# Performance work log

Measured on AMD Instinct MI355X. Metric: run time of the kernel, lower is better.

## Reference

```python
import jax, jax.numpy as jnp
import numpy as np

N, E = 50000, 600000
D_IN = 128; D_HID = 128; D_OUT = 128
HEADS = 4; HD = D_HID // HEADS  # per-head dim (32); also edge-encoder output dim
EDGE_DIM = 64


def _w(key, shape, scale=0.05):
    return jax.random.normal(key, shape, dtype=jnp.float32) * scale


def setup_inputs() -> dict:
    key = jax.random.key(0)
    ks = jax.random.split(key, 20)
    return {
        "x": jax.random.normal(ks[0], (N, D_IN), dtype=jnp.float32),
        "edge_index": jax.random.randint(ks[1], (2, E), 0, N),
        "edge_attr": jax.random.normal(ks[2], (E, EDGE_DIM), dtype=jnp.float32),
        # edge feature encoders: Linear(EDGE_DIM, HD), one per GNN layer
        "ew0": _w(ks[3], (EDGE_DIM, HD)), "eb0": jnp.zeros((HD,), jnp.float32),
        "ew1": _w(ks[4], (EDGE_DIM, HD)), "eb1": jnp.zeros((HD,), jnp.float32),
        # ordered-message-passing attention: Linear(dim, 1) per layer
        "ow0": _w(ks[5], (D_IN, 1)), "ob0": jnp.zeros((1,), jnp.float32),
        "ow1": _w(ks[6], (D_OUT, 1)), "ob1": jnp.zeros((1,), jnp.float32),
        # GATConv layer 0: in=D_IN, heads=HEADS, per-head out=HD, edge_dim=HD
        "g0_W": _w(ks[7], (D_IN, HEADS * HD)),
        "g0_as": _w(ks[8], (HEADS, HD)), "g0_ad": _w(ks[9], (HEADS, HD)),
        "g0_We": _w(ks[10], (HD, HEADS * HD)), "g0_ae": _w(ks[11], (HEADS, HD)),
        "g0_b": jnp.zeros((HEADS * HD,), jnp.float32),
        # GATConv layer 1 (final): in=HEADS*HD, heads=1, out=D_OUT, edge_dim=HD
        "g1_W": _w(ks[12], (HEADS * HD, D_OUT)),
        "g1_as": _w(ks[13], (1, D_OUT)), "g1_ad": _w(ks[14], (1, D_OUT)),
        "g1_We": _w(ks[15], (HD, D_OUT)), "g1_ae": _w(ks[16], (1, D_OUT)),
        "g1_b": jnp.zeros((D_OUT,), jnp.float32),
    }


def _gat_conv(x, src, dst, e_attr, W, a_src, a_dst, We, a_e, bias):
    """PyG GATConv with edge features, add_self_loops=True, fill_value='mean'."""
    H, C = a_src.shape
    n = x.shape[0]
    # self-loop edge_attr = per-dst mean of incoming edge_attr (PyG fill_value='mean')
    ones = jnp.ones((src.shape[0],), x.dtype)
    cnt = jax.ops.segment_sum(ones, dst, num_segments=n)
    loop_attr = jax.ops.segment_sum(e_attr, dst, num_segments=n) / jnp.maximum(cnt, 1.0)[:, None]
    loop = jnp.arange(n)
    src2 = jnp.concatenate([src, loop])
    dst2 = jnp.concatenate([dst, loop])
    ea2 = jnp.concatenate([e_attr, loop_attr], axis=0)  # [E+N, HD]
    xs = (x @ W).reshape(n, H, C)                       # [N, H, C]
    al_src = jnp.einsum('nhc,hc->nh', xs, a_src)
    al_dst = jnp.einsum('nhc,hc->nh', xs, a_dst)
    ee = (ea2 @ We).reshape(-1, H, C)                   # [E+N, H, C]
    al_e = jnp.einsum('ehc,hc->eh', ee, a_e)
    alpha = jax.nn.leaky_relu(al_src[src2] + al_dst[dst2] + al_e, 0.2)  # [E+N, H]
    # segment softmax over edges sharing a destination node
    mx = jax.ops.segment_max(alpha, dst2, num_segments=n)
    ex = jnp.exp(alpha - mx[dst2])
    den = jax.ops.segment_sum(ex, dst2, num_segments=n)
    coef = ex / (den[dst2] + 1e-16)
    out = jax.ops.segment_sum(xs[src2] * coef[..., None], dst2, num_segments=n)
    return out.reshape(n, H * C) + bias


def reference(x, edge_index, edge_attr, ew0, eb0, ew1, eb1, ow0, ob0, ow1, ob1,
              g0_W, g0_as, g0_ad, g0_We, g0_ae, g0_b,
              g1_W, g1_as, g1_ad, g1_We, g1_ae, g1_b):
    src, dst = edge_index[0], edge_index[1]
    original_x = x
    layers = [
        (ew0, eb0, ow0, ob0, g0_W, g0_as, g0_ad, g0_We, g0_ae, g0_b),
        (ew1, eb1, ow1, ob1, g1_W, g1_as, g1_ad, g1_We, g1_ae, g1_b),
    ]
    for i, (ew, eb, ow, ob, W, a_s, a_d, We, a_e, b) in enumerate(layers):
        te = jax.nn.relu(edge_attr @ ew + eb)            # [E, HD]
        score = (x @ ow + ob)[:, 0]                       # [N] order-attention scores
        te = te * jnp.exp(score)[src][:, None]            # ordered message weighting
        x_new = _gat_conv(x, src, dst, te, W, a_s, a_d, We, a_e, b)
        x = x_new + x if x.shape[-1] == x_new.shape[-1] else x_new
        if i < len(layers) - 1:
            x = jax.nn.relu(x)  # dropout p=0.0 in eval
    if original_x.shape[-1] == x.shape[-1]:
        x = x + original_x
    return x
```

## Files before the change

### kernel.cpp

```cpp
#include <hip/hip_runtime.h>
#include <math.h>

#define D 128
#define ED 64
#define HD 32

typedef short s16x8 __attribute__((ext_vector_type(8)));
typedef unsigned short u16x8 __attribute__((ext_vector_type(8)));
typedef float f32x4 __attribute__((ext_vector_type(4)));

static __device__ inline unsigned short f2b(float f) {
  unsigned int u = __float_as_uint(f);
  unsigned int r = (u + 0x7fff + ((u >> 16) & 1)) >> 16;
  return (unsigned short)r;
}
static __device__ inline float b2f(unsigned short b) {
  return __uint_as_float(((unsigned int)b) << 16);
}

__global__ __launch_bounds__(256)
void count_prep_kernel(const int* __restrict__ dst, int* __restrict__ cnt,
                       int* __restrict__ rank, int E, int egrid,
                       const float* __restrict__ g0W, unsigned short* __restrict__ Wt0,
                       const float* __restrict__ g1W, unsigned short* __restrict__ Wt1,
                       const float* __restrict__ ew0, unsigned short* __restrict__ ewt0,
                       const float* __restrict__ ew1, unsigned short* __restrict__ ewt1,
                       const float* __restrict__ g0We, const float* __restrict__ g0ae,
                       float* __restrict__ M0,
                       const float* __restrict__ g1We, const float* __restrict__ g1ae,
                       float* __restrict__ M1) {
  int b = blockIdx.x, t = threadIdx.x;
  if (b < egrid) {
    int e = b * 256 + t;
    if (e < E) rank[e] = atomicAdd(&cnt[dst[e]], 1);
    return;
  }
  int pb = b - egrid;
  if (pb < 128) {
    const float* W = pb < 64 ? g0W : g1W;
    unsigned short* Wt = pb < 64 ? Wt0 : Wt1;
    int id = (pb & 63) * 256 + t;
    int nn = id >> 7, k = id & 127;
    Wt[id] = f2b(W[k * D + nn]);
  } else if (pb < 144) {
    const float* ew = pb < 136 ? ew0 : ew1;
    unsigned short* ewt = pb < 136 ? ewt0 : ewt1;
    int id = ((pb - 128) & 7) * 256 + t;
    if (id < HD * ED) {
      int i = id >> 6, k = id & 63;
      int ch = (i < 16) ? ((i >> 2) * 8 + (i & 3))
                        : (((i - 16) >> 2) * 8 + 4 + ((i - 16) & 3));
      ewt[id] = f2b(ew[k * HD + ch]);
    }
  } else if (pb == 144) {
    if (t < HD * 4) {
      int d = t >> 2, h = t & 3;
      float s = 0.f;
      for (int c = 0; c < 32; ++c) s += g0We[d * D + h * 32 + c] * g0ae[h * 32 + c];
      M0[t] = s;
    }
  } else {
    if (t < HD) {
      float s = 0.f;
      for (int c = 0; c < D; ++c) s += g1We[t * D + c] * g1ae[c];
      M1[t] = s;
    }
  }
}

__global__ __launch_bounds__(256)
void scan_a_kernel(const int* __restrict__ cnt, int* __restrict__ bsum, int n) {
  __shared__ int sh[256];
  int t = threadIdx.x;
  int i = blockIdx.x * 256 + t;
  sh[t] = (i < n) ? cnt[i] : 0;
  __syncthreads();
  for (int off = 128; off >= 1; off >>= 1) {
    if (t < off) sh[t] += sh[t + off];
    __syncthreads();
  }
  if (t == 0) bsum[blockIdx.x] = sh[0];
}

__global__ __launch_bounds__(256)
void scan_b_kernel(const int* __restrict__ bsum, int* __restrict__ boff, int nb,
                   int* __restrict__ rowptr_n, int E) {
  __shared__ int sh[256];
  int t = threadIdx.x;
  int v = (t < nb) ? bsum[t] : 0;
  sh[t] = v;
  __syncthreads();
  for (int off = 1; off < 256; off <<= 1) {
    int add = (t >= off) ? sh[t - off] : 0;
    __syncthreads();
    sh[t] += add;
    __syncthreads();
  }
  if (t < nb) boff[t] = sh[t] - v;
  if (t == 0) *rowptr_n = E;
}

__global__ __launch_bounds__(256)
void scan_c_kernel(const int* __restrict__ cnt, const int* __restrict__ boff,
                   int* __restrict__ rowptr, int n) {
  __shared__ int sh[256];
  int t = threadIdx.x;
  int i = blockIdx.x * 256 + t;
  int v = (i < n) ? cnt[i] : 0;
  sh[t] = v;
  __syncthreads();
  for (int off = 1; off < 256; off <<= 1) {
    int add = (t >= off) ? sh[t - off] : 0;
    __syncthreads();
    sh[t] += add;
    __syncthreads();
  }
  if (i < n) rowptr[i] = boff[blockIdx.x] + sh[t] - v;
}

template<int H, bool INBF16>
static __device__ void gemm_body(int gblk, int tid, const void* xin,
                                 const unsigned short* __restrict__ Wt,
                                 const float* __restrict__ a_s, const float* __restrict__ a_d,
                                 const float* __restrict__ ow, const float* __restrict__ ob,
                                 unsigned short* __restrict__ xs, float* __restrict__ al_src,
                                 float* __restrict__ al_dst, float* __restrict__ escore,
                                 float2* __restrict__ als1, int n) {
  int wave = tid >> 6;
  int lane = tid & 63;
  int q = lane >> 4;
  int l16 = lane & 15;
  int base = gblk * 64 + wave * 16;
  int rowRaw = base + l16;
  int row = rowRaw < n ? rowRaw : n - 1;
  s16x8 a[4];
  float scp = 0.f;
  if (INBF16) {
    const unsigned short* xrow = (const unsigned short*)xin + (size_t)row * D;
#pragma unroll
    for (int kk = 0; kk < 4; ++kk) {
      int kb = kk * 32 + q * 8;
      u16x8 v = *(const u16x8*)(xrow + kb);
      float4 o0 = *(const float4*)(ow + kb);
      float4 o1 = *(const float4*)(ow + kb + 4);
      scp += b2f(v[0]) * o0.x + b2f(v[1]) * o0.y + b2f(v[2]) * o0.z + b2f(v[3]) * o0.w
           + b2f(v[4]) * o1.x + b2f(v[5]) * o1.y + b2f(v[6]) * o1.z + b2f(v[7]) * o1.w;
      a[kk] = *(const s16x8*)&v;
    }
  } else {
    const float* xrow = (const float*)xin + (size_t)row * D;
#pragma unroll
    for (int kk = 0; kk < 4; ++kk) {
      int kb = kk * 32 + q * 8;
      float4 v0 = *(const float4*)(xrow + kb);
      float4 v1 = *(const float4*)(xrow + kb + 4);
      float4 o0 = *(const float4*)(ow + kb);
      float4 o1 = *(const float4*)(ow + kb + 4);
      scp += v0.x * o0.x + v0.y * o0.y + v0.z * o0.z + v0.w * o0.w
           + v1.x * o1.x + v1.y * o1.y + v1.z * o1.z + v1.w * o1.w;
      s16x8 t;
      t[0] = (short)f2b(v0.x); t[1] = (short)f2b(v0.y);
      t[2] = (short)f2b(v0.z); t[3] = (short)f2b(v0.w);
      t[4] = (short)f2b(v1.x); t[5] = (short)f2b(v1.y);
      t[6] = (short)f2b(v1.z); t[7] = (short)f2b(v1.w);
      a[kk] = t;
    }
  }
  scp += __shfl_xor(scp, 16);
  scp += __shfl_xor(scp, 32);
  if (H == 4) {
    if (q == 0 && rowRaw < n) escore[rowRaw] = __expf(scp + ob[0]);
  }

  f32x4 acc[8];
#pragma unroll
  for (int nf = 0; nf < 8; ++nf) { f32x4 z = {0.f, 0.f, 0.f, 0.f}; acc[nf] = z; }
#pragma unroll
  for (int kk = 0; kk < 4; ++kk) {
    int kb = kk * 32 + q * 8;
#pragma unroll
    for (int nf = 0; nf < 8; ++nf) {
      s16x8 b = *(const s16x8*)(Wt + (size_t)(nf * 16 + l16) * D + kb);
      acc[nf] = __builtin_amdgcn_mfma_f32_16x16x32_bf16(a[kk], b, acc[nf], 0, 0, 0);
    }
  }
#pragma unroll
  for (int nf = 0; nf < 8; ++nf) {
#pragma unroll
    for (int r = 0; r < 4; ++r) {
      int rr = base + q * 4 + r;
      if (rr < n) xs[(size_t)rr * D + nf * 16 + l16] = f2b(acc[nf][r]);
    }
  }
  float asv[8], adv[8];
#pragma unroll
  for (int nf = 0; nf < 8; ++nf) { asv[nf] = a_s[nf * 16 + l16]; adv[nf] = a_d[nf * 16 + l16]; }
  if (H == 4) {
    float mys = 0.f, myd = 0.f;
#pragma unroll
    for (int r = 0; r < 4; ++r) {
#pragma unroll
      for (int h = 0; h < 4; ++h) {
        float vs = acc[2 * h][r] * asv[2 * h] + acc[2 * h + 1][r] * asv[2 * h + 1];
        float vd = acc[2 * h][r] * adv[2 * h] + acc[2 * h + 1][r] * adv[2 * h + 1];
        vs += __shfl_xor(vs, 1); vd += __shfl_xor(vd, 1);
        vs += __shfl_xor(vs, 2); vd += __shfl_xor(vd, 2);
        vs += __shfl_xor(vs, 4); vd += __shfl_xor(vd, 4);
        vs += __shfl_xor(vs, 8); vd += __shfl_xor(vd, 8);
        if (l16 == r * 4 + h) { mys = vs; myd = vd; }
      }
    }
    int orow = base + q * 4 + (l16 >> 2);
    if (orow < n) {
      al_src[(size_t)orow * 4 + (l16 & 3)] = mys;
      al_dst[(size_t)orow * 4 + (l16 & 3)] = myd;
    }
  } else {
    float mys = 0.f, myd = 0.f;
#pragma unroll
    for (int r = 0; r < 4; ++r) {
      float vs = 0.f, vd = 0.f;
#pragma unroll
      for (int nf = 0; nf < 8; ++nf) { vs = fmaf(acc[nf][r], asv[nf], vs); vd = fmaf(acc[nf][r], adv[nf], vd); }
      vs += __shfl_xor(vs, 1); vd += __shfl_xor(vd, 1);
      vs += __shfl_xor(vs, 2); vd += __shfl_xor(vd, 2);
      vs += __shfl_xor(vs, 4); vd += __shfl_xor(vd, 4);
      vs += __shfl_xor(vs, 8); vd += __shfl_xor(vd, 8);
      if (l16 == r) { mys = vs; myd = vd; }
    }
    float scr = __shfl(scp, q * 4 + l16);
    int orow = base + q * 4 + l16;
    if (l16 < 4 && orow < n) {
      al_dst[orow] = myd;
      als1[orow] = make_float2(mys, __expf(scr + ob[0]));
    }
  }
}

__global__ __launch_bounds__(256)
void fill_gemm_kernel(const int* __restrict__ src, const int* __restrict__ dst,
                      const int* __restrict__ rowptr, const int* __restrict__ rank,
                      int2* __restrict__ slotmap, int E, int fgrid,
                      const float* __restrict__ x, const unsigned short* __restrict__ Wt0,
                      const float* __restrict__ g0as, const float* __restrict__ g0ad,
                      const float* __restrict__ ow0, const float* __restrict__ ob0,
                      unsigned short* __restrict__ xs, float* __restrict__ al_src,
                      float* __restrict__ al_dst, float* __restrict__ escore, int n) {
  if ((int)blockIdx.x < fgrid) {
    int e = blockIdx.x * 256 + threadIdx.x;
    if (e < E) {
      int d = dst[e];
      slotmap[rowptr[d] + rank[e]] = make_int2(e, src[e]);
    }
  } else {
    gemm_body<4, false>(blockIdx.x - fgrid, threadIdx.x, x, Wt0, g0as, g0ad, ow0, ob0,
                        xs, al_src, al_dst, escore, nullptr, n);
  }
}

__global__ __launch_bounds__(256)
void gemm1_kernel(const unsigned short* __restrict__ x1b, const unsigned short* __restrict__ Wt,
                  const float* __restrict__ a_s, const float* __restrict__ a_d,
                  const float* __restrict__ ow, const float* __restrict__ ob,
                  unsigned short* __restrict__ xs, float* __restrict__ al_dst,
                  float2* __restrict__ als1, int n) {
  gemm_body<1, true>(blockIdx.x, threadIdx.x, x1b, Wt, a_s, a_d, ow, ob,
                     xs, nullptr, al_dst, nullptr, als1, n);
}

__global__ __launch_bounds__(256)
void edge_csr_kernel(const int2* __restrict__ slotmap,
                     const float* __restrict__ ea,
                     const unsigned short* __restrict__ ewt0p,
                     const unsigned short* __restrict__ ewt1p,
                     const float* __restrict__ eb0, const float* __restrict__ eb1,
                     const float* __restrict__ M0, const float* __restrict__ M1,
                     const float* __restrict__ escore0,
                     float* __restrict__ alef0,
                     float* __restrict__ ale1raw,
                     int E) {
  int wave = threadIdx.x >> 6, lane = threadIdx.x & 63;
  int q = lane >> 4, l16 = lane & 15;
  int ebase = (blockIdx.x * 4 + wave) * 64;
  if (ebase >= E) return;
  s16x8 a0l0 = *(const s16x8*)(ewt0p + l16 * 64 + q * 8);
  s16x8 a0l1 = *(const s16x8*)(ewt0p + l16 * 64 + 32 + q * 8);
  s16x8 a0h0 = *(const s16x8*)(ewt0p + (16 + l16) * 64 + q * 8);
  s16x8 a0h1 = *(const s16x8*)(ewt0p + (16 + l16) * 64 + 32 + q * 8);
  s16x8 a1l0 = *(const s16x8*)(ewt1p + l16 * 64 + q * 8);
  s16x8 a1l1 = *(const s16x8*)(ewt1p + l16 * 64 + 32 + q * 8);
  s16x8 a1h0 = *(const s16x8*)(ewt1p + (16 + l16) * 64 + q * 8);
  s16x8 a1h1 = *(const s16x8*)(ewt1p + (16 + l16) * 64 + 32 + q * 8);
  float4 b0lo = *(const float4*)(eb0 + q * 8);
  float4 b0hi = *(const float4*)(eb0 + q * 8 + 4);
  float4 b1lo = *(const float4*)(eb1 + q * 8);
  float4 b1hi = *(const float4*)(eb1 + q * 8 + 4);
  s16x8 mf0, mf1;
#pragma unroll
  for (int j = 0; j < 8; ++j) {
    mf0[j] = (l16 < 4) ? (short)f2b(M0[(q * 8 + j) * 4 + l16]) : (short)0;
    mf1[j] = (l16 == 0) ? (short)f2b(M1[q * 8 + j]) : (short)0;
  }
  int el = ebase + lane;
  int elc = el < E ? el : E - 1;
  int2 sm = slotmap[elc];
  int eo = sm.x;
  float esc = escore0[sm.y];

#pragma unroll
  for (int st = 0; st < 4; ++st) {
    int slot16 = st * 16 + l16;
    int e16 = ebase + slot16;
    int row = __shfl(eo, slot16);
    const float* er = ea + (size_t)row * ED;
    float4 u0 = *(const float4*)(er + q * 8);
    float4 u1 = *(const float4*)(er + q * 8 + 4);
    float4 u2 = *(const float4*)(er + 32 + q * 8);
    float4 u3 = *(const float4*)(er + 32 + q * 8 + 4);
    s16x8 bk0, bk1;
    bk0[0] = (short)f2b(u0.x); bk0[1] = (short)f2b(u0.y);
    bk0[2] = (short)f2b(u0.z); bk0[3] = (short)f2b(u0.w);
    bk0[4] = (short)f2b(u1.x); bk0[5] = (short)f2b(u1.y);
    bk0[6] = (short)f2b(u1.z); bk0[7] = (short)f2b(u1.w);
    bk1[0] = (short)f2b(u2.x); bk1[1] = (short)f2b(u2.y);
    bk1[2] = (short)f2b(u2.z); bk1[3] = (short)f2b(u2.w);
    bk1[4] = (short)f2b(u3.x); bk1[5] = (short)f2b(u3.y);
    bk1[6] = (short)f2b(u3.z); bk1[7] = (short)f2b(u3.w);
    f32x4 zl0 = {0.f,0.f,0.f,0.f}, zh0 = {0.f,0.f,0.f,0.f};
    f32x4 zl1 = {0.f,0.f,0.f,0.f}, zh1 = {0.f,0.f,0.f,0.f};
    zl0 = __builtin_amdgcn_mfma_f32_16x16x32_bf16(a0l0, bk0, zl0, 0, 0, 0);
    zl0 = __builtin_amdgcn_mfma_f32_16x16x32_bf16(a0l1, bk1, zl0, 0, 0, 0);
    zh0 = __builtin_amdgcn_mfma_f32_16x16x32_bf16(a0h0, bk0, zh0, 0, 0, 0);
    zh0 = __builtin_amdgcn_mfma_f32_16x16x32_bf16(a0h1, bk1, zh0, 0, 0, 0);
    zl1 = __builtin_amdgcn_mfma_f32_16x16x32_bf16(a1l0, bk0, zl1, 0, 0, 0);
    zl1 = __builtin_amdgcn_mfma_f32_16x16x32_bf16(a1l1, bk1, zl1, 0, 0, 0);
    zh1 = __builtin_amdgcn_mfma_f32_16x16x32_bf16(a1h0, bk0, zh1, 0, 0, 0);
    zh1 = __builtin_amdgcn_mfma_f32_16x16x32_bf16(a1h1, bk1, zh1, 0, 0, 0);
    s16x8 zb0, zb1;
    zb0[0] = (short)f2b(fmaxf(zl0[0] + b0lo.x, 0.f));
    zb0[1] = (short)f2b(fmaxf(zl0[1] + b0lo.y, 0.f));
    zb0[2] = (short)f2b(fmaxf(zl0[2] + b0lo.z, 0.f));
    zb0[3] = (short)f2b(fmaxf(zl0[3] + b0lo.w, 0.f));
    zb0[4] = (short)f2b(fmaxf(zh0[0] + b0hi.x, 0.f));
    zb0[5] = (short)f2b(fmaxf(zh0[1] + b0hi.y, 0.f));
    zb0[6] = (short)f2b(fmaxf(zh0[2] + b0hi.z, 0.f));
    zb0[7] = (short)f2b(fmaxf(zh0[3] + b0hi.w, 0.f));
    zb1[0] = (short)f2b(fmaxf(zl1[0] + b1lo.x, 0.f));
    zb1[1] = (short)f2b(fmaxf(zl1[1] + b1lo.y, 0.f));
    zb1[2] = (short)f2b(fmaxf(zl1[2] + b1lo.z, 0.f));
    zb1[3] = (short)f2b(fmaxf(zl1[3] + b1lo.w, 0.f));
    zb1[4] = (short)f2b(fmaxf(zh1[0] + b1hi.x, 0.f));
    zb1[5] = (short)f2b(fmaxf(zh1[1] + b1hi.y, 0.f));
    zb1[6] = (short)f2b(fmaxf(zh1[2] + b1hi.z, 0.f));
    zb1[7] = (short)f2b(fmaxf(zh1[3] + b1hi.w, 0.f));
    f32x4 r0 = {0.f,0.f,0.f,0.f}, r1 = {0.f,0.f,0.f,0.f};
    r0 = __builtin_amdgcn_mfma_f32_16x16x32_bf16(mf0, zb0, r0, 0, 0, 0);
    r1 = __builtin_amdgcn_mfma_f32_16x16x32_bf16(mf1, zb1, r1, 0, 0, 0);
    float esc_e = __shfl(esc, slot16);
    if (q == 0 && e16 < E) {
      *(float4*)(alef0 + (size_t)e16 * 4) =
          make_float4(r0[0] * esc_e, r0[1] * esc_e, r0[2] * esc_e, r0[3] * esc_e);
      ale1raw[e16] = r1[0];
    }
  }
}

template<int H, bool RELU, bool ADD_ORIG, bool INBF16, bool OUTBF16>
__global__ __launch_bounds__(256)
void agg_kernel(const int* __restrict__ rowptr, const int2* __restrict__ slotmap,
                const unsigned short* __restrict__ xs, const float* __restrict__ alef,
                const float* __restrict__ al_src, const float* __restrict__ al_dst,
                const float2* __restrict__ als1,
                const float* __restrict__ bias, const void* __restrict__ xin,
                const float* __restrict__ orig, void* __restrict__ outv, int n) {
  int wid = blockIdx.x * 4 + (threadIdx.x >> 6);
  int lane = threadIdx.x & 63;
  if (wid >= n) return;
  int half = lane >> 5;
  int l32 = lane & 31;
  int h0 = (H == 4) ? (l32 >> 3) : 0;
  const ushort4* xs4 = (const ushort4*)xs;
  float adst = al_dst[(size_t)wid * H + h0];
  float ax0 = 0.f, ax1 = 0.f, ax2 = 0.f, ax3 = 0.f, den = 0.f, sale = 0.f;
  int b = rowptr[wid], e = rowptr[wid + 1];
  int m = e - b;

#define EDGE_ACC(I_)                                                     \
  {                                                                      \
    int idx_ = (I_);                                                     \
    bool v_ = idx_ < e;                                                  \
    int ic_ = v_ ? idx_ : b;                                             \
    int s_ = slotmap[ic_].y;                                             \
    float al_, ev_;                                                      \
    if (H == 4) {                                                        \
      al_ = alef[(size_t)ic_ * 4 + h0];                                  \
      float aa_ = al_src[(size_t)s_ * 4 + h0] + adst + al_;              \
      ev_ = __expf(aa_ > 0.f ? aa_ : 0.2f * aa_);                        \
    } else {                                                             \
      float2 ae_ = als1[s_];                                             \
      al_ = alef[ic_] * ae_.y;                                           \
      float aa_ = ae_.x + adst + al_;                                    \
      ev_ = __expf(aa_ > 0.f ? aa_ : 0.2f * aa_);                        \
    }                                                                    \
    if (!v_) { ev_ = 0.f; al_ = 0.f; }                                   \
    ushort4 u_ = xs4[(size_t)s_ * 32 + l32];                             \
    ax0 = fmaf(ev_, b2f(u_.x), ax0); ax1 = fmaf(ev_, b2f(u_.y), ax1);    \
    ax2 = fmaf(ev_, b2f(u_.z), ax2); ax3 = fmaf(ev_, b2f(u_.w), ax3);    \
    den += ev_; sale += al_;                                             \
  }

  for (int k = 0; k < m; k += 8) {
    int i0 = b + k + half;
    EDGE_ACC(i0)
    EDGE_ACC(i0 + 2)
    EDGE_ACC(i0 + 4)
    EDGE_ACC(i0 + 6)
  }
#undef EDGE_ACC

  ax0 += __shfl_xor(ax0, 32); ax1 += __shfl_xor(ax1, 32);
  ax2 += __shfl_xor(ax2, 32); ax3 += __shfl_xor(ax3, 32);
  den += __shfl_xor(den, 32); sale += __shfl_xor(sale, 32);

  float la = sale / (float)(m > 1 ? m : 1);
  float asrc_w = (H == 4) ? al_src[(size_t)wid * 4 + h0] : als1[wid].x;
  float a = asrc_w + adst + la;
  float lr = a > 0.f ? a : 0.2f * a;
  float evl = __expf(lr);
  ushort4 us = xs4[(size_t)wid * 32 + l32];
  ax0 = fmaf(evl, b2f(us.x), ax0); ax1 = fmaf(evl, b2f(us.y), ax1);
  ax2 = fmaf(evl, b2f(us.z), ax2); ax3 = fmaf(evl, b2f(us.w), ax3);
  float dinv = 1.f / (den + evl + 1e-16f);
  if (half == 0) {
    float4 bi = ((const float4*)bias)[l32];
    float o0 = ax0 * dinv + bi.x;
    float o1 = ax1 * dinv + bi.y;
    float o2 = ax2 * dinv + bi.z;
    float o3 = ax3 * dinv + bi.w;
    if (INBF16) {
      ushort4 xi = ((const ushort4*)xin)[(size_t)wid * 32 + l32];
      o0 += b2f(xi.x); o1 += b2f(xi.y); o2 += b2f(xi.z); o3 += b2f(xi.w);
    } else {
      float4 xi = ((const float4*)xin)[(size_t)wid * 32 + l32];
      o0 += xi.x; o1 += xi.y; o2 += xi.z; o3 += xi.w;
    }
    if (ADD_ORIG) {
      float4 og = ((const float4*)orig)[(size_t)wid * 32 + l32];
      o0 += og.x; o1 += og.y; o2 += og.z; o3 += og.w;
    }
    if (RELU) {
      o0 = fmaxf(o0, 0.f); o1 = fmaxf(o1, 0.f);
      o2 = fmaxf(o2, 0.f); o3 = fmaxf(o3, 0.f);
    }
    if (OUTBF16) {
      ushort4 ob;
      ob.x = f2b(o0); ob.y = f2b(o1); ob.z = f2b(o2); ob.w = f2b(o3);
      ((ushort4*)outv)[(size_t)wid * 32 + l32] = ob;
    } else {
      ((float4*)outv)[(size_t)wid * 32 + l32] = make_float4(o0, o1, o2, o3);
    }
  }
}

extern "C" void kernel_launch(void* const* d_in, const int* in_sizes, int n_in,
                              void* d_out, int out_size, void* d_ws, size_t ws_size,
                              hipStream_t stream) {
  const float* x   = (const float*)d_in[0];
  const int*   ei  = (const int*)d_in[1];
  const float* ea  = (const float*)d_in[2];
  const float* ew0 = (const float*)d_in[3];
  const float* eb0 = (const float*)d_in[4];
  const float* ew1 = (const float*)d_in[5];
  const float* eb1 = (const float*)d_in[6];
  const float* ow0 = (const float*)d_in[7];
  const float* ob0 = (const float*)d_in[8];
  const float* ow1 = (const float*)d_in[9];
  const float* ob1 = (const float*)d_in[10];
  const float* g0W = (const float*)d_in[11];
  const float* g0as= (const float*)d_in[12];
  const float* g0ad= (const float*)d_in[13];
  const float* g0We= (const float*)d_in[14];
  const float* g0ae= (const float*)d_in[15];
  const float* g0b = (const float*)d_in[16];
  const float* g1W = (const float*)d_in[17];
  const float* g1as= (const float*)d_in[18];
  const float* g1ad= (const float*)d_in[19];
  const float* g1We= (const float*)d_in[20];
  const float* g1ae= (const float*)d_in[21];
  const float* g1b = (const float*)d_in[22];
  float* out = (float*)d_out;

  const int N = in_sizes[0] / D;
  const int E = in_sizes[1] / 2;
  const int* srcp = ei;
  const int* dstp = ei + E;

  char* w = (char*)d_ws;
  size_t off = 0;
  auto alloc = [&](size_t bytes) {
    void* p = w + off;
    off += (bytes + 255) & ~(size_t)255;
    return p;
  };
  size_t Nb = ((size_t)N * 4 + 255) & ~(size_t)255;
  int*   cnt     = (int*)alloc(Nb);
  int*   rank    = (int*)alloc((size_t)E * 4);
  unsigned short* xs   = (unsigned short*)alloc((size_t)N * D * 2);
  unsigned short* x1b  = (unsigned short*)alloc((size_t)N * D * 2);
  float* alef0   = (float*)alloc((size_t)E * 4 * 4);
  float* ale1raw = (float*)alloc((size_t)E * 4);
  float* al_src  = (float*)alloc((size_t)N * 4 * 4);
  float* al_dst  = (float*)alloc((size_t)N * 4 * 4);
  float* escore  = (float*)alloc((size_t)N * 4);
  float2* als1   = (float2*)alloc((size_t)N * 8);
  float* M0      = (float*)alloc(HD * 4 * 4);
  float* M1      = (float*)alloc(HD * 4);
  unsigned short* Wt0 = (unsigned short*)alloc((size_t)D * D * 2);
  unsigned short* Wt1 = (unsigned short*)alloc((size_t)D * D * 2);
  unsigned short* ewt0 = (unsigned short*)alloc((size_t)HD * ED * 2);
  unsigned short* ewt1 = (unsigned short*)alloc((size_t)HD * ED * 2);
  int*   rowptr  = (int*)alloc((size_t)(N + 1) * 4);
  int2*  slotmap = (int2*)alloc((size_t)E * 8);
  int*   bsum    = (int*)alloc(1024);
  int*   boff    = (int*)alloc(1024);

  int egrid  = (E + 255) / 256;
  int ngrid4 = (N + 3) / 4;
  int ggrid  = (N + 63) / 64;
  int nsb    = (N + 255) / 256;

  hipMemsetAsync(cnt, 0, Nb, stream);
  count_prep_kernel<<<egrid + 146, 256, 0, stream>>>(dstp, cnt, rank, E, egrid,
                                                     g0W, Wt0, g1W, Wt1,
                                                     ew0, ewt0, ew1, ewt1,
                                                     g0We, g0ae, M0, g1We, g1ae, M1);
  scan_a_kernel<<<nsb, 256, 0, stream>>>(cnt, bsum, N);
  scan_b_kernel<<<1, 256, 0, stream>>>(bsum, boff, nsb, rowptr + N, E);
  scan_c_kernel<<<nsb, 256, 0, stream>>>(cnt, boff, rowptr, N);
  fill_gemm_kernel<<<egrid + ggrid, 256, 0, stream>>>(srcp, dstp, rowptr, rank,
                                                      slotmap, E, egrid,
                                                      x, Wt0, g0as, g0ad, ow0, ob0,
                                                      xs, al_src, al_dst, escore, N);
  edge_csr_kernel<<<egrid, 256, 0, stream>>>(slotmap, ea, ewt0, ewt1,
                                             eb0, eb1, M0, M1, escore,
                                             alef0, ale1raw, E);
  agg_kernel<4, true, false, false, true><<<ngrid4, 256, 0, stream>>>(
      rowptr, slotmap, xs, alef0, al_src, al_dst, nullptr,
      g0b, x, nullptr, x1b, N);
  gemm1_kernel<<<ggrid, 256, 0, stream>>>(x1b, Wt1, g1as, g1ad, ow1, ob1,
                                          xs, al_dst, als1, N);
  agg_kernel<1, false, true, true, false><<<ngrid4, 256, 0, stream>>>(
      rowptr, slotmap, xs, ale1raw, nullptr, al_dst, als1,
      g1b, x1b, x, out, N);
}
```

Measured before the change: 222.9 us.

## Fuse CSR fill, layer-0 GEMM and edge encoder into one kernel

Moves the layer-0 order-attention score computation into the count/prep kernel so it is ready earlier. The edge encoder then processes edges in original order, reading src directly instead of going through the slotmap. That removes its dependency on the CSR fill and lets it be merged with the fill and GEMM into a single launch. The aggregation kernel now looks up per-edge attention values through the original edge id stored in slotmap, which adds one indirect gather per edge there. In exchange it saves a kernel launch and allows the edge_attr rows to be read sequentially.

Result: slower. 233.8 us (+4.9%).

```diff
diff --git a/kernel.cpp b/kernel.cpp
--- a/kernel.cpp
+++ b/kernel.cpp
@@ -28,7 +28,9 @@
                        const float* __restrict__ g0We, const float* __restrict__ g0ae,
                        float* __restrict__ M0,
                        const float* __restrict__ g1We, const float* __restrict__ g1ae,
-                       float* __restrict__ M1) {
+                       float* __restrict__ M1,
+                       const float* __restrict__ x, const float* __restrict__ ow0,
+                       const float* __restrict__ ob0, float* __restrict__ escore, int n) {
   int b = blockIdx.x, t = threadIdx.x;
   if (b < egrid) {
     int e = b * 256 + t;
@@ -59,11 +61,21 @@
       for (int c = 0; c < 32; ++c) s += g0We[d * D + h * 32 + c] * g0ae[h * 32 + c];
       M0[t] = s;
     }
-  } else {
+  } else if (pb == 145) {
     if (t < HD) {
       float s = 0.f;
       for (int c = 0; c < D; ++c) s += g1We[t * D + c] * g1ae[c];
       M1[t] = s;
+    }
+  } else {
+    int node = (pb - 146) * 4 + (t >> 6);
+    int lane = t & 63;
+    if (node < n) {
+      const float* xr = x + (size_t)node * D;
+      float s = xr[lane] * ow0[lane] + xr[64 + lane] * ow0[64 + lane];
+#pragma unroll
+      for (int off = 32; off >= 1; off >>= 1) s += __shfl_xor(s, off);
+      if (lane == 0) escore[node] = __expf(s + ob0[0]);
     }
   }
 }
@@ -124,7 +136,7 @@
                                  const float* __restrict__ a_s, const float* __restrict__ a_d,
                                  const float* __restrict__ ow, const float* __restrict__ ob,
                                  unsigned short* __restrict__ xs, float* __restrict__ al_src,
-                                 float* __restrict__ al_dst, float* __restrict__ escore,
+                                 float* __restrict__ al_dst,
                                  float2* __restrict__ als1, int n) {
   int wave = tid >> 6;
   int lane = tid & 63;
@@ -141,10 +153,12 @@
     for (int kk = 0; kk < 4; ++kk) {
       int kb = kk * 32 + q * 8;
       u16x8 v = *(const u16x8*)(xrow + kb);
-      float4 o0 = *(const float4*)(ow + kb);
-      float4 o1 = *(const float4*)(ow + kb + 4);
-      scp += b2f(v[0]) * o0.x + b2f(v[1]) * o0.y + b2f(v[2]) * o0.z + b2f(v[3]) * o0.w
-           + b2f(v[4]) * o1.x + b2f(v[5]) * o1.y + b2f(v[6]) * o1.z + b2f(v[7]) * o1.w;
+      if (H == 1) {
+        float4 o0 = *(const float4*)(ow + kb);
+        float4 o1 = *(const float4*)(ow + kb + 4);
+        scp += b2f(v[0]) * o0.x + b2f(v[1]) * o0.y + b2f(v[2]) * o0.z + b2f(v[3]) * o0.w
+             + b2f(v[4]) * o1.x + b2f(v[5]) * o1.y + b2f(v[6]) * o1.z + b2f(v[7]) * o1.w;
+      }
       a[kk] = *(const s16x8*)&v;
     }
   } else {
@@ -154,10 +168,12 @@
       int kb = kk * 32 + q * 8;
       float4 v0 = *(const float4*)(xrow + kb);
       float4 v1 = *(const float4*)(xrow + kb + 4);
-      float4 o0 = *(const float4*)(ow + kb);
-      float4 o1 = *(const float4*)(ow + kb + 4);
-      scp += v0.x * o0.x + v0.y * o0.y + v0.z * o0.z + v0.w * o0.w
-           + v1.x * o1.x + v1.y * o1.y + v1.z * o1.z + v1.w * o1.w;
+      if (H == 1) {
+        float4 o0 = *(const float4*)(ow + kb);
+        float4 o1 = *(const float4*)(ow + kb + 4);
+        scp += v0.x * o0.x + v0.y * o0.y + v0.z * o0.z + v0.w * o0.w
+             + v1.x * o1.x + v1.y * o1.y + v1.z * o1.z + v1.w * o1.w;
+      }
       s16x8 t;
       t[0] = (short)f2b(v0.x); t[1] = (short)f2b(v0.y);
       t[2] = (short)f2b(v0.z); t[3] = (short)f2b(v0.w);
@@ -166,10 +182,9 @@
       a[kk] = t;
     }
   }
-  scp += __shfl_xor(scp, 16);
-  scp += __shfl_xor(scp, 32);
-  if (H == 4) {
-    if (q == 0 && rowRaw < n) escore[rowRaw] = __expf(scp + ob[0]);
+  if (H == 1) {
+    scp += __shfl_xor(scp, 16);
+    scp += __shfl_xor(scp, 32);
   }
 
   f32x4 acc[8];
@@ -237,51 +252,20 @@
   }
 }
 
-__global__ __launch_bounds__(256)
-void fill_gemm_kernel(const int* __restrict__ src, const int* __restrict__ dst,
-                      const int* __restrict__ rowptr, const int* __restrict__ rank,
-                      int2* __restrict__ slotmap, int E, int fgrid,
-                      const float* __restrict__ x, const unsigned short* __restrict__ Wt0,
-                      const float* __restrict__ g0as, const float* __restrict__ g0ad,
-                      const float* __restrict__ ow0, const float* __restrict__ ob0,
-                      unsigned short* __restrict__ xs, float* __restrict__ al_src,
-                      float* __restrict__ al_dst, float* __restrict__ escore, int n) {
-  if ((int)blockIdx.x < fgrid) {
-    int e = blockIdx.x * 256 + threadIdx.x;
-    if (e < E) {
-      int d = dst[e];
-      slotmap[rowptr[d] + rank[e]] = make_int2(e, src[e]);
-    }
-  } else {
-    gemm_body<4, false>(blockIdx.x - fgrid, threadIdx.x, x, Wt0, g0as, g0ad, ow0, ob0,
-                        xs, al_src, al_dst, escore, nullptr, n);
-  }
-}
-
-__global__ __launch_bounds__(256)
-void gemm1_kernel(const unsigned short* __restrict__ x1b, const unsigned short* __restrict__ Wt,
-                  const float* __restrict__ a_s, const float* __restrict__ a_d,
-                  const float* __restrict__ ow, const float* __restrict__ ob,
-                  unsigned short* __restrict__ xs, float* __restrict__ al_dst,
-                  float2* __restrict__ als1, int n) {
-  gemm_body<1, true>(blockIdx.x, threadIdx.x, x1b, Wt, a_s, a_d, ow, ob,
-                     xs, nullptr, al_dst, nullptr, als1, n);
-}
-
-__global__ __launch_bounds__(256)
-void edge_csr_kernel(const int2* __restrict__ slotmap,
-                     const float* __restrict__ ea,
-                     const unsigned short* __restrict__ ewt0p,
-                     const unsigned short* __restrict__ ewt1p,
-                     const float* __restrict__ eb0, const float* __restrict__ eb1,
-                     const float* __restrict__ M0, const float* __restrict__ M1,
-                     const float* __restrict__ escore0,
-                     float* __restrict__ alef0,
-                     float* __restrict__ ale1raw,
-                     int E) {
-  int wave = threadIdx.x >> 6, lane = threadIdx.x & 63;
+static __device__ void edge_body(int eblk, int tid,
+                                 const int* __restrict__ src,
+                                 const float* __restrict__ ea,
+                                 const unsigned short* __restrict__ ewt0p,
+                                 const unsigned short* __restrict__ ewt1p,
+                                 const float* __restrict__ eb0, const float* __restrict__ eb1,
+                                 const float* __restrict__ M0, const float* __restrict__ M1,
+                                 const float* __restrict__ escore0,
+                                 float* __restrict__ alef0,
+                                 float* __restrict__ ale1raw,
+                                 int E) {
+  int wave = tid >> 6, lane = tid & 63;
   int q = lane >> 4, l16 = lane & 15;
-  int ebase = (blockIdx.x * 4 + wave) * 64;
+  int ebase = (eblk * 4 + wave) * 64;
   if (ebase >= E) return;
   s16x8 a0l0 = *(const s16x8*)(ewt0p + l16 * 64 + q * 8);
   s16x8 a0l1 = *(const s16x8*)(ewt0p + l16 * 64 + 32 + q * 8);
@@ -303,16 +287,14 @@
   }
   int el = ebase + lane;
   int elc = el < E ? el : E - 1;
-  int2 sm = slotmap[elc];
-  int eo = sm.x;
-  float esc = escore0[sm.y];
+  float esc = escore0[src[elc]];
 
 #pragma unroll
   for (int st = 0; st < 4; ++st) {
     int slot16 = st * 16 + l16;
     int e16 = ebase + slot16;
-    int row = __shfl(eo, slot16);
-    const float* er = ea + (size_t)row * ED;
+    int ec = e16 < E ? e16 : E - 1;
+    const float* er = ea + (size_t)ec * ED;
     float4 u0 = *(const float4*)(er + q * 8);
     float4 u1 = *(const float4*)(er + q * 8 + 4);
     float4 u2 = *(const float4*)(er + 32 + q * 8);
@@ -365,6 +347,47 @@
   }
 }
 
+__global__ __launch_bounds__(256)
+void mega_kernel(const int* __restrict__ src, const int* __restrict__ dst,
+                 const int* __restrict__ rowptr, const int* __restrict__ rank,
+                 int2* __restrict__ slotmap, int E, int fgrid, int ggrid,
+                 const float* __restrict__ x, const unsigned short* __restrict__ Wt0,
+                 const float* __restrict__ g0as, const float* __restrict__ g0ad,
+                 unsigned short* __restrict__ xs, float* __restrict__ al_src,
+                 float* __restrict__ al_dst, int n,
+                 const float* __restrict__ ea,
+                 const unsigned short* __restrict__ ewt0p,
+                 const unsigned short* __restrict__ ewt1p,
+                 const float* __restrict__ eb0, const float* __restrict__ eb1,
+                 const float* __restrict__ M0, const float* __restrict__ M1,
+                 const float* __restrict__ escore,
+                 float* __restrict__ alef0, float* __restrict__ ale1raw) {
+  int b = blockIdx.x;
+  if (b < fgrid) {
+    int e = b * 256 + threadIdx.x;
+    if (e < E) {
+      int d = dst[e];
+      slotmap[rowptr[d] + rank[e]] = make_int2(e, src[e]);
+    }
+  } else if (b < fgrid + ggrid) {
+    gemm_body<4, false>(b - fgrid, threadIdx.x, x, Wt0, g0as, g0ad, nullptr, nullptr,
+                        xs, al_src, al_dst, nullptr, n);
+  } else {
+    edge_body(b - fgrid - ggrid, threadIdx.x, src, ea, ewt0p, ewt1p,
+              eb0, eb1, M0, M1, escore, alef0, ale1raw, E);
+  }
+}
+
+__global__ __launch_bounds__(256)
+void gemm1_kernel(const unsigned short* __restrict__ x1b, const unsigned short* __restrict__ Wt,
+                  const float* __restrict__ a_s, const float* __restrict__ a_d,
+                  const float* __restrict__ ow, const float* __restrict__ ob,
+                  unsigned short* __restrict__ xs, float* __restrict__ al_dst,
+                  float2* __restrict__ als1, int n) {
+  gemm_body<1, true>(blockIdx.x, threadIdx.x, x1b, Wt, a_s, a_d, ow, ob,
+                     xs, nullptr, al_dst, als1, n);
+}
+
 template<int H, bool RELU, bool ADD_ORIG, bool INBF16, bool OUTBF16>
 __global__ __launch_bounds__(256)
 void agg_kernel(const int* __restrict__ rowptr, const int2* __restrict__ slotmap,
@@ -390,15 +413,17 @@
     int idx_ = (I_);                                                     \
     bool v_ = idx_ < e;                                                  \
     int ic_ = v_ ? idx_ : b;                                             \
-    int s_ = slotmap[ic_].y;                                             \
+    int2 sm_ = slotmap[ic_];                                             \
+    int s_ = sm_.y;                                                      \
+    int eo_ = sm_.x;                                                     \
     float al_, ev_;                                                      \
     if (H == 4) {                                                        \
-      al_ = alef[(size_t)ic_ * 4 + h0];                                  \
+      al_ = alef[(size_t)eo_ * 4 + h0];                                  \
       float aa_ = al_src[(size_t)s_ * 4 + h0] + adst + al_;              \
       ev_ = __expf(aa_ > 0.f ? aa_ : 0.2f * aa_);                        \
     } else {                                                             \
       float2 ae_ = als1[s_];                                             \
-      al_ = alef[ic_] * ae_.y;                                           \
+      al_ = alef[eo_] * ae_.y;                                           \
       float aa_ = ae_.x + adst + al_;                                    \
       ev_ = __expf(aa_ > 0.f ? aa_ : 0.2f * aa_);                        \
     }                                                                    \
@@ -530,20 +555,18 @@
   int nsb    = (N + 255) / 256;
 
   hipMemsetAsync(cnt, 0, Nb, stream);
-  count_prep_kernel<<<egrid + 146, 256, 0, stream>>>(dstp, cnt, rank, E, egrid,
-                                                     g0W, Wt0, g1W, Wt1,
-                                                     ew0, ewt0, ew1, ewt1,
-                                                     g0We, g0ae, M0, g1We, g1ae, M1);
+  count_prep_kernel<<<egrid + 146 + ngrid4, 256, 0, stream>>>(
+      dstp, cnt, rank, E, egrid,
+      g0W, Wt0, g1W, Wt1, ew0, ewt0, ew1, ewt1,
+      g0We, g0ae, M0, g1We, g1ae, M1,
+      x, ow0, ob0, escore, N);
   scan_a_kernel<<<nsb, 256, 0, stream>>>(cnt, bsum, N);
   scan_b_kernel<<<1, 256, 0, stream>>>(bsum, boff, nsb, rowptr + N, E);
   scan_c_kernel<<<nsb, 256, 0, stream>>>(cnt, boff, rowptr, N);
-  fill_gemm_kernel<<<egrid + ggrid, 256, 0, stream>>>(srcp, dstp, rowptr, rank,
-                                                      slotmap, E, egrid,
-                                                      x, Wt0, g0as, g0ad, ow0, ob0,
-                                                      xs, al_src, al_dst, escore, N);
-  edge_csr_kernel<<<egrid, 256, 0, stream>>>(slotmap, ea, ewt0, ewt1,
-                                             eb0, eb1, M0, M1, escore,
-                                             alef0, ale1raw, E);
+  mega_kernel<<<egrid + ggrid + egrid, 256, 0, stream>>>(
+      srcp, dstp, rowptr, rank, slotmap, E, egrid, ggrid,
+      x, Wt0, g0as, g0ad, xs, al_src, al_dst, N,
+      ea, ewt0, ewt1, eb0, eb1, M0, M1, escore, alef0, ale1raw);
   agg_kernel<4, true, false, false, true><<<ngrid4, 256, 0, stream>>>(
       rowptr, slotmap, xs, alef0, al_src, al_dst, nullptr,
       g0b, x, nullptr, x1b, N);
```
